# Optimization experiments

Hardware: AMD Instinct MI355X
Metric: run time of the kernel (lower is better)

The kernel has to match this reference:

```python
import jax, jax.numpy as jnp
import numpy as np

D_MODEL, D_K, D_V = 1024, 64, 64
B, S = 4, 4096

def setup_inputs() -> dict:
    key = jax.random.key(0)
    ks = jax.random.split(key, 9)
    s_in = 1.0 / np.sqrt(D_MODEL)
    return {
        "Q": jax.random.normal(ks[0], (B, S, D_MODEL), jnp.float32),
        "K": jax.random.normal(ks[1], (B, S, D_MODEL), jnp.float32),
        "V": jax.random.normal(ks[2], (B, S, D_MODEL), jnp.float32),
        "Wq": jax.random.uniform(ks[3], (D_MODEL, D_K), jnp.float32, -s_in, s_in),
        "bq": jax.random.uniform(ks[4], (D_K,), jnp.float32, -s_in, s_in),
        "Wk": jax.random.uniform(ks[5], (D_MODEL, D_K), jnp.float32, -s_in, s_in),
        "bk": jax.random.uniform(ks[6], (D_K,), jnp.float32, -s_in, s_in),
        "Wv": jax.random.uniform(ks[7], (D_MODEL, D_V), jnp.float32, -s_in, s_in),
        "bv": jax.random.uniform(ks[8], (D_V,), jnp.float32, -s_in, s_in),
    }

def reference(Q, K, V, Wq, bq, Wk, bk, Wv, bv):
    # Linear projections: [B,S,d_model] -> [B,S,d_k/d_v]
    q = jnp.einsum("bsm,mk->bsk", Q, Wq) + bq
    k = jnp.einsum("btm,mk->btk", K, Wk) + bk
    v = jnp.einsum("btm,mv->btv", V, Wv) + bv
    # Scaled dot-product attention, softmax over key axis (dim=2)
    scores = jnp.einsum("bsk,btk->bst", q, k) / jnp.sqrt(jnp.float32(D_K))
    attn = jax.nn.softmax(scores, axis=2)  # [B,S,S]
    return jnp.einsum("bst,btv->bsv", attn, v)
```

## Files before the change

### kernel.cpp

```cpp
#include <hip/hip_runtime.h>

typedef __bf16 bf16;
typedef __attribute__((ext_vector_type(4))) __bf16 bf16x4;
typedef __attribute__((ext_vector_type(8))) __bf16 bf16x8;
typedef __attribute__((ext_vector_type(4))) float f32x4;
typedef __attribute__((ext_vector_type(16))) float f32x16;

#define MFMA16(a, b, c) __builtin_amdgcn_mfma_f32_16x16x32_bf16((a), (b), (c), 0, 0, 0)
#define MFMA32(a, b, c) __builtin_amdgcn_mfma_f32_32x32x16_bf16((a), (b), (c), 0, 0, 0)

__device__ __forceinline__ bf16 tobf(float f) {
    unsigned u = __float_as_uint(f);
    u += 0x7fffu + ((u >> 16) & 1u);
    unsigned short h = (unsigned short)(u >> 16);
    bf16 r;
    __builtin_memcpy(&r, &h, 2);
    return r;
}

__global__ void wconv_kernel(const float* __restrict__ Wq, const float* __restrict__ Wk,
                             const float* __restrict__ Wv, bf16* __restrict__ Wt) {
    int j = blockIdx.y;
    const float* W = (j == 0) ? Wq : ((j == 1) ? Wk : Wv);
    int idx = blockIdx.x * 256 + threadIdx.x;
    int m = idx >> 6, n = idx & 63;
    Wt[(size_t)j * 65536 + (size_t)n * 1024 + m] = tobf(W[idx]);
}

__launch_bounds__(256, 3)
__global__ void proj_kernel(const float* __restrict__ Q, const float* __restrict__ K,
                            const float* __restrict__ V, const bf16* __restrict__ Wt,
                            const float* __restrict__ bq, const float* __restrict__ bk,
                            const float* __restrict__ bv,
                            bf16* __restrict__ q_ws, bf16* __restrict__ k_ws,
                            bf16* __restrict__ vT_ws) {
    const int j = blockIdx.y;
    const float* In   = (j == 0) ? Q : ((j == 1) ? K : V);
    const float* bias = (j == 0) ? bq : ((j == 1) ? bk : bv);
    const bf16* W = Wt + (size_t)j * 65536;

    __shared__ bf16 As[64][136];
    __shared__ bf16 Bs[64][136];

    const int tid = threadIdx.x;
    const int wave = tid >> 6, lane = tid & 63;
    const int quad = lane >> 4, l16 = lane & 15;
    const int rbase = blockIdx.x * 64;

    int arow[8], ag[8];
    const float* apt[8];
#pragma unroll
    for (int i = 0; i < 8; i++) {
        int u = i * 256 + tid;
        arow[i] = u >> 5; ag[i] = u & 31;
        apt[i] = In + (size_t)(rbase + arow[i]) * 1024 + ag[i] * 4;
    }
    int brow[4], bg[4];
    const bf16* bpt[4];
#pragma unroll
    for (int i = 0; i < 4; i++) {
        int u = i * 256 + tid;
        brow[i] = u >> 4; bg[i] = u & 15;
        bpt[i] = W + (size_t)brow[i] * 1024 + bg[i] * 8;
    }

    f32x4 abuf[8];
    bf16x8 bbuf[4];
#pragma unroll
    for (int i = 0; i < 8; i++) abuf[i] = *(const f32x4*)(apt[i]);
#pragma unroll
    for (int i = 0; i < 4; i++) bbuf[i] = *(const bf16x8*)(bpt[i]);

    f32x4 acc[4];
#pragma unroll
    for (int nt = 0; nt < 4; nt++) acc[nt] = {0.f, 0.f, 0.f, 0.f};

#pragma unroll
    for (int it = 0; it < 8; it++) {
#pragma unroll
        for (int i = 0; i < 8; i++) {
            bf16x4 c;
            c[0] = (bf16)abuf[i][0]; c[1] = (bf16)abuf[i][1];
            c[2] = (bf16)abuf[i][2]; c[3] = (bf16)abuf[i][3];
            *(bf16x4*)&As[arow[i]][ag[i] * 4] = c;
        }
#pragma unroll
        for (int i = 0; i < 4; i++) *(bf16x8*)&Bs[brow[i]][bg[i] * 8] = bbuf[i];

        if (it < 7) {
            int kn = (it + 1) * 128;
#pragma unroll
            for (int i = 0; i < 8; i++) abuf[i] = *(const f32x4*)(apt[i] + kn);
#pragma unroll
            for (int i = 0; i < 4; i++) bbuf[i] = *(const bf16x8*)(bpt[i] + kn);
        }
        __syncthreads();

        const int r = wave * 16 + l16;
#pragma unroll
        for (int c = 0; c < 4; c++) {
            bf16x8 av = *(const bf16x8*)&As[r][c * 32 + quad * 8];
#pragma unroll
            for (int nt = 0; nt < 4; nt++) {
                bf16x8 bv = *(const bf16x8*)&Bs[nt * 16 + l16][c * 32 + quad * 8];
                acc[nt] = MFMA16(av, bv, acc[nt]);
            }
        }
        __syncthreads();
    }

    const float scale = (j == 0) ? 0.125f * 1.44269504088896f : 1.0f;

    if (j != 2) {
        bf16* dst = (j == 0) ? q_ws : k_ws;
#pragma unroll
        for (int nt = 0; nt < 4; nt++) {
            int n = nt * 16 + l16;
            float bb = bias[n];
#pragma unroll
            for (int r4 = 0; r4 < 4; r4++) {
                int row = rbase + wave * 16 + quad * 4 + r4;
                dst[(size_t)row * 64 + n] = tobf((acc[nt][r4] + bb) * scale);
            }
        }
    } else {
        bf16 (*vtile)[72] = (bf16(*)[72])As;
#pragma unroll
        for (int nt = 0; nt < 4; nt++) {
            int n = nt * 16 + l16;
            float bb = bias[n];
#pragma unroll
            for (int r4 = 0; r4 < 4; r4++) {
                vtile[n][wave * 16 + quad * 4 + r4] = tobf(acc[nt][r4] + bb);
            }
        }
        __syncthreads();
        int bi = rbase >> 12, t0 = rbase & 4095;
        int d = tid >> 2, part = (tid & 3) * 16;
        bf16x8 x0 = *(const bf16x8*)&vtile[d][part];
        bf16x8 x1 = *(const bf16x8*)&vtile[d][part + 8];
        bf16* dst = vT_ws + (size_t)(bi * 64 + d) * 4096 + t0 + part;
        *(bf16x8*)dst = x0;
        *(bf16x8*)(dst + 8) = x1;
    }
}

__launch_bounds__(256, 4)
__global__ void attn_kernel(const bf16* __restrict__ q_ws, const bf16* __restrict__ k_ws,
                            const bf16* __restrict__ vT_ws,
                            float* __restrict__ po, float* __restrict__ pl,
                            float* __restrict__ out, int keys_per_split, int direct) {
    const int b = blockIdx.z, split = blockIdx.y;
    const int tid = threadIdx.x, wave = tid >> 6, lane = tid & 63;
    const int l32 = lane & 31, h = lane >> 5;
    const int sw = l32 & 7;

    __shared__ bf16 kt[64][64];
    __shared__ bf16 vt[64][64];
    __shared__ bf16 pt[4][32][64];

    const int qrow0 = b * 4096 + blockIdx.x * 128 + wave * 32;

    bf16x8 qf[4];
    const bf16* qp = q_ws + (size_t)(qrow0 + l32) * 64 + h * 8;
#pragma unroll
    for (int c = 0; c < 4; c++) qf[c] = *(const bf16x8*)(qp + c * 16);

    f32x16 o0, o1;
    float l_lane = 0.f;
#pragma unroll
    for (int i = 0; i < 16; i++) { o0[i] = 0.f; o1[i] = 0.f; }

    const int key0 = split * keys_per_split;
    const int srow = tid >> 3;
    const int sg = tid & 7;
    const int sgk = sg ^ (srow & 7);
    const bf16* kg = k_ws + (size_t)(b * 4096 + key0 + srow) * 64 + sg * 8;
    const bf16* vg = vT_ws + (size_t)(b * 64 + srow) * 4096 + key0 + sg * 8;

    uint4 kv0 = *(const uint4*)kg;
    uint4 kv1 = *(const uint4*)(kg + 2048);
    uint4 vv0 = *(const uint4*)vg;
    uint4 vv1 = *(const uint4*)(vg + 131072);

    for (int t0 = 0; t0 < keys_per_split; t0 += 64) {
        __syncthreads();
        *(uint4*)&kt[srow][sgk * 8]      = kv0;
        *(uint4*)&kt[srow + 32][sgk * 8] = kv1;
        *(uint4*)&vt[srow][sgk * 8]      = vv0;
        *(uint4*)&vt[srow + 32][sgk * 8] = vv1;
        if (t0 + 64 < keys_per_split) {
            kv0 = *(const uint4*)(kg + (size_t)(t0 + 64) * 64);
            kv1 = *(const uint4*)(kg + (size_t)(t0 + 64) * 64 + 2048);
            vv0 = *(const uint4*)(vg + t0 + 64);
            vv1 = *(const uint4*)(vg + t0 + 64 + 131072);
        }
        __syncthreads();

#pragma unroll
        for (int kt32 = 0; kt32 < 2; kt32++) {
            f32x16 s;
#pragma unroll
            for (int i = 0; i < 16; i++) s[i] = 0.f;
#pragma unroll
            for (int c = 0; c < 4; c++) {
                bf16x8 kf = *(const bf16x8*)(&kt[kt32 * 32 + l32][((2 * c + h) ^ sw) * 8]);
                s = MFMA32(kf, qf[c], s);
            }
#pragma unroll
            for (int g = 0; g < 4; g++) {
                float p0 = __builtin_amdgcn_exp2f(s[4 * g + 0]);
                float p1 = __builtin_amdgcn_exp2f(s[4 * g + 1]);
                float p2 = __builtin_amdgcn_exp2f(s[4 * g + 2]);
                float p3 = __builtin_amdgcn_exp2f(s[4 * g + 3]);
                l_lane += (p0 + p1) + (p2 + p3);
                bf16x4 pk;
                pk[0] = (bf16)p0; pk[1] = (bf16)p1; pk[2] = (bf16)p2; pk[3] = (bf16)p3;
                int gp = (kt32 * 4 + g) ^ sw;
                *(bf16x4*)(&pt[wave][l32][gp * 8 + 4 * h]) = pk;
            }
        }

#pragma unroll
        for (int tc = 0; tc < 4; tc++) {
            int gp = ((2 * tc + h) ^ sw) * 8;
            bf16x8 pf  = *(const bf16x8*)(&pt[wave][l32][gp]);
            bf16x8 vf0 = *(const bf16x8*)(&vt[l32][gp]);
            bf16x8 vf1 = *(const bf16x8*)(&vt[32 + l32][gp]);
            o0 = MFMA32(pf, vf0, o0);
            o1 = MFMA32(pf, vf1, o1);
        }
    }

    l_lane += __shfl_xor(l_lane, 32);

    if (direct) {
        float* orow = out + (size_t)qrow0 * 64;
#pragma unroll
        for (int i = 0; i < 16; i++) {
            int R = (i & 3) + 8 * (i >> 2) + 4 * h;
            float inv = 1.0f / __shfl(l_lane, R);
            orow[(size_t)R * 64 + l32]      = o0[i] * inv;
            orow[(size_t)R * 64 + 32 + l32] = o1[i] * inv;
        }
    } else {
        size_t prow = (size_t)split * 16384 + qrow0;
        float* pob = po + prow * 64;
#pragma unroll
        for (int i = 0; i < 16; i++) {
            int R = (i & 3) + 8 * (i >> 2) + 4 * h;
            pob[(size_t)R * 64 + l32]      = o0[i];
            pob[(size_t)R * 64 + 32 + l32] = o1[i];
        }
        if (h == 0) pl[prow + l32] = l_lane;
    }
}

__launch_bounds__(256)
__global__ void combine_kernel(const float* __restrict__ po, const float* __restrict__ pl,
                               float* __restrict__ out, int nsplit) {
    int idx = blockIdx.x * 256 + threadIdx.x;
    int row = idx >> 6;
    float so = 0.f, sl = 0.f;
    for (int s = 0; s < nsplit; s++) {
        so += po[(size_t)s * 1048576 + idx];
        sl += pl[(size_t)s * 16384 + row];
    }
    out[idx] = so / sl;
}

extern "C" void kernel_launch(void* const* d_in, const int* in_sizes, int n_in,
                              void* d_out, int out_size, void* d_ws, size_t ws_size,
                              hipStream_t stream) {
    const float* Q  = (const float*)d_in[0];
    const float* K  = (const float*)d_in[1];
    const float* V  = (const float*)d_in[2];
    const float* Wq = (const float*)d_in[3];
    const float* bq = (const float*)d_in[4];
    const float* Wk = (const float*)d_in[5];
    const float* bk = (const float*)d_in[6];
    const float* Wv = (const float*)d_in[7];
    const float* bv = (const float*)d_in[8];
    float* out = (float*)d_out;

    char* ws = (char*)d_ws;
    bf16* Wt    = (bf16*)ws;
    bf16* q_ws  = (bf16*)(ws + 393216);
    bf16* k_ws  = (bf16*)(ws + 393216 + 2097152);
    bf16* vT_ws = (bf16*)(ws + 393216 + 2 * 2097152);
    const size_t base = 393216 + 3 * 2097152;

    const size_t per_split = 16384u * 4u + 1048576u * 4u;
    int nsplit = 1;
    if (ws_size >= base + 8 * per_split) nsplit = 8;
    else if (ws_size >= base + 4 * per_split) nsplit = 4;
    else if (ws_size >= base + 2 * per_split) nsplit = 2;

    float* pl = (float*)(ws + base);
    float* po = (float*)(ws + base + (size_t)nsplit * 65536);

    hipLaunchKernelGGL(wconv_kernel, dim3(256, 3), dim3(256), 0, stream, Wq, Wk, Wv, Wt);
    hipLaunchKernelGGL(proj_kernel, dim3(256, 3), dim3(256), 0, stream,
                       Q, K, V, Wt, bq, bk, bv, q_ws, k_ws, vT_ws);
    hipLaunchKernelGGL(attn_kernel, dim3(32, nsplit, 4), dim3(256), 0, stream,
                       q_ws, k_ws, vT_ws, po, pl, out, 4096 / nsplit, nsplit == 1 ? 1 : 0);
    if (nsplit > 1) {
        hipLaunchKernelGGL(combine_kernel, dim3(4096), dim3(256), 0, stream, po, pl, out, nsplit);
    }
}
```

Before: 246.3 us.

## Load projection A operand straight into MFMA registers and double-buffer weights

In the projection kernel, each lane now loads its own fp32 input row slice from global memory, converts it to bf16 and feeds it directly to the MFMA. The activation tile no longer goes through shared memory. The weight tile is double-buffered in LDS, so one barrier per k-iteration can be dropped. The launch-bounds occupancy hint rises from 3 to 4. This cuts LDS traffic and barrier stalls, at the cost of less regular global access patterns and tighter register pressure.

```diff
diff --git a/kernel.cpp b/kernel.cpp
--- a/kernel.cpp
+++ b/kernel.cpp
@@ -27,7 +27,7 @@
     Wt[(size_t)j * 65536 + (size_t)n * 1024 + m] = tobf(W[idx]);
 }
 
-__launch_bounds__(256, 3)
+__launch_bounds__(256, 4)
 __global__ void proj_kernel(const float* __restrict__ Q, const float* __restrict__ K,
                             const float* __restrict__ V, const bf16* __restrict__ Wt,
                             const float* __restrict__ bq, const float* __restrict__ bk,
@@ -39,22 +39,16 @@
     const float* bias = (j == 0) ? bq : ((j == 1) ? bk : bv);
     const bf16* W = Wt + (size_t)j * 65536;
 
-    __shared__ bf16 As[64][136];
-    __shared__ bf16 Bs[64][136];
+    __shared__ bf16 Bs[2][64][136];
 
     const int tid = threadIdx.x;
     const int wave = tid >> 6, lane = tid & 63;
     const int quad = lane >> 4, l16 = lane & 15;
     const int rbase = blockIdx.x * 64;
-
-    int arow[8], ag[8];
-    const float* apt[8];
-#pragma unroll
-    for (int i = 0; i < 8; i++) {
-        int u = i * 256 + tid;
-        arow[i] = u >> 5; ag[i] = u & 31;
-        apt[i] = In + (size_t)(rbase + arow[i]) * 1024 + ag[i] * 4;
-    }
+    const int myrow = rbase + wave * 16 + l16;
+
+    const float* abase = In + (size_t)myrow * 1024 + quad * 8;
+
     int brow[4], bg[4];
     const bf16* bpt[4];
 #pragma unroll
@@ -64,49 +58,57 @@
         bpt[i] = W + (size_t)brow[i] * 1024 + bg[i] * 8;
     }
 
-    f32x4 abuf[8];
+    f32x4 an[8];
+#pragma unroll
+    for (int c = 0; c < 4; c++) {
+        an[2 * c]     = *(const f32x4*)(abase + c * 32);
+        an[2 * c + 1] = *(const f32x4*)(abase + c * 32 + 4);
+    }
     bf16x8 bbuf[4];
 #pragma unroll
-    for (int i = 0; i < 8; i++) abuf[i] = *(const f32x4*)(apt[i]);
-#pragma unroll
     for (int i = 0; i < 4; i++) bbuf[i] = *(const bf16x8*)(bpt[i]);
 
     f32x4 acc[4];
 #pragma unroll
     for (int nt = 0; nt < 4; nt++) acc[nt] = {0.f, 0.f, 0.f, 0.f};
 
+    bf16x8 acur[4];
+
 #pragma unroll
     for (int it = 0; it < 8; it++) {
 #pragma unroll
-        for (int i = 0; i < 8; i++) {
-            bf16x4 c;
-            c[0] = (bf16)abuf[i][0]; c[1] = (bf16)abuf[i][1];
-            c[2] = (bf16)abuf[i][2]; c[3] = (bf16)abuf[i][3];
-            *(bf16x4*)&As[arow[i]][ag[i] * 4] = c;
-        }
-#pragma unroll
-        for (int i = 0; i < 4; i++) *(bf16x8*)&Bs[brow[i]][bg[i] * 8] = bbuf[i];
-
+        for (int c = 0; c < 4; c++) {
+            bf16x8 v;
+            v[0] = (bf16)an[2 * c][0];     v[1] = (bf16)an[2 * c][1];
+            v[2] = (bf16)an[2 * c][2];     v[3] = (bf16)an[2 * c][3];
+            v[4] = (bf16)an[2 * c + 1][0]; v[5] = (bf16)an[2 * c + 1][1];
+            v[6] = (bf16)an[2 * c + 1][2]; v[7] = (bf16)an[2 * c + 1][3];
+            acur[c] = v;
+        }
         if (it < 7) {
-            int kn = (it + 1) * 128;
-#pragma unroll
-            for (int i = 0; i < 8; i++) abuf[i] = *(const f32x4*)(apt[i] + kn);
-#pragma unroll
-            for (int i = 0; i < 4; i++) bbuf[i] = *(const bf16x8*)(bpt[i] + kn);
+            const float* ap = abase + (it + 1) * 128;
+#pragma unroll
+            for (int c = 0; c < 4; c++) {
+                an[2 * c]     = *(const f32x4*)(ap + c * 32);
+                an[2 * c + 1] = *(const f32x4*)(ap + c * 32 + 4);
+            }
+        }
+#pragma unroll
+        for (int i = 0; i < 4; i++) *(bf16x8*)&Bs[it & 1][brow[i]][bg[i] * 8] = bbuf[i];
+        if (it < 7) {
+#pragma unroll
+            for (int i = 0; i < 4; i++) bbuf[i] = *(const bf16x8*)(bpt[i] + (it + 1) * 128);
         }
         __syncthreads();
 
-        const int r = wave * 16 + l16;
 #pragma unroll
         for (int c = 0; c < 4; c++) {
-            bf16x8 av = *(const bf16x8*)&As[r][c * 32 + quad * 8];
 #pragma unroll
             for (int nt = 0; nt < 4; nt++) {
-                bf16x8 bv = *(const bf16x8*)&Bs[nt * 16 + l16][c * 32 + quad * 8];
-                acc[nt] = MFMA16(av, bv, acc[nt]);
-            }
-        }
-        __syncthreads();
+                bf16x8 bv = *(const bf16x8*)&Bs[it & 1][nt * 16 + l16][c * 32 + quad * 8];
+                acc[nt] = MFMA16(acur[c], bv, acc[nt]);
+            }
+        }
     }
 
     const float scale = (j == 0) ? 0.125f * 1.44269504088896f : 1.0f;
@@ -124,7 +126,7 @@
             }
         }
     } else {
-        bf16 (*vtile)[72] = (bf16(*)[72])As;
+        bf16 (*vtile)[72] = (bf16(*)[72])Bs;
 #pragma unroll
         for (int nt = 0; nt < 4; nt++) {
             int n = nt * 16 + l16;
```

Measured after the change: 243.6 us. About the same (-1.1%).

## Stream projection inputs into double-buffered swizzled LDS via global_load_lds

Applied to the files above, without the earlier changes.

The projection kernel no longer loads fp32 inputs into registers, converts them and writes bf16 to LDS. It now copies fp32 tiles straight into a double-buffered, XOR-swizzled LDS area with global_load_lds, prefetching the next K slice while the current one is computed, and converts to bf16 when reading fragments. Weight fragments are read directly from global/L2 instead of being staged in LDS. This aims to overlap the memory-bound input stream with compute and cut register and VALU staging work. In exchange it uses more LDS per block and issues more global weight loads. Correctness depends on the barrier waiting for the async LDS loads.

```diff
diff --git a/kernel.cpp b/kernel.cpp
--- a/kernel.cpp
+++ b/kernel.cpp
@@ -16,6 +16,12 @@
     bf16 r;
     __builtin_memcpy(&r, &h, 2);
     return r;
+}
+
+__device__ __forceinline__ void stage16(const void* g, void* l) {
+    __builtin_amdgcn_global_load_lds(
+        (const __attribute__((address_space(1))) unsigned int*)g,
+        (__attribute__((address_space(3))) unsigned int*)l, 16, 0, 0);
 }
 
 __global__ void wconv_kernel(const float* __restrict__ Wq, const float* __restrict__ Wk,
@@ -39,72 +45,66 @@
     const float* bias = (j == 0) ? bq : ((j == 1) ? bk : bv);
     const bf16* W = Wt + (size_t)j * 65536;
 
-    __shared__ bf16 As[64][136];
-    __shared__ bf16 Bs[64][136];
+    __shared__ float As[2][64][64];
 
     const int tid = threadIdx.x;
     const int wave = tid >> 6, lane = tid & 63;
     const int quad = lane >> 4, l16 = lane & 15;
     const int rbase = blockIdx.x * 64;
 
-    int arow[8], ag[8];
-    const float* apt[8];
-#pragma unroll
-    for (int i = 0; i < 8; i++) {
-        int u = i * 256 + tid;
-        arow[i] = u >> 5; ag[i] = u & 31;
-        apt[i] = In + (size_t)(rbase + arow[i]) * 1024 + ag[i] * 4;
-    }
-    int brow[4], bg[4];
-    const bf16* bpt[4];
+    const char* asrc[4];
+    char* adst0[4];
+    char* adst1[4];
 #pragma unroll
     for (int i = 0; i < 4; i++) {
         int u = i * 256 + tid;
-        brow[i] = u >> 4; bg[i] = u & 15;
-        bpt[i] = W + (size_t)brow[i] * 1024 + bg[i] * 8;
-    }
-
-    f32x4 abuf[8];
-    bf16x8 bbuf[4];
-#pragma unroll
-    for (int i = 0; i < 8; i++) abuf[i] = *(const f32x4*)(apt[i]);
-#pragma unroll
-    for (int i = 0; i < 4; i++) bbuf[i] = *(const bf16x8*)(bpt[i]);
+        int row = u >> 4;
+        int rg = ((u & 15) * 16) ^ ((row & 7) << 4);
+        asrc[i] = (const char*)(In + (size_t)(rbase + row) * 1024) + rg;
+        adst0[i] = (char*)&As[0][0][0] + u * 16;
+        adst1[i] = (char*)&As[1][0][0] + u * 16;
+    }
+
+#pragma unroll
+    for (int i = 0; i < 4; i++) stage16(asrc[i], adst0[i]);
+    __syncthreads();
 
     f32x4 acc[4];
 #pragma unroll
     for (int nt = 0; nt < 4; nt++) acc[nt] = {0.f, 0.f, 0.f, 0.f};
 
-#pragma unroll
-    for (int it = 0; it < 8; it++) {
-#pragma unroll
-        for (int i = 0; i < 8; i++) {
-            bf16x4 c;
-            c[0] = (bf16)abuf[i][0]; c[1] = (bf16)abuf[i][1];
-            c[2] = (bf16)abuf[i][2]; c[3] = (bf16)abuf[i][3];
-            *(bf16x4*)&As[arow[i]][ag[i] * 4] = c;
-        }
-#pragma unroll
-        for (int i = 0; i < 4; i++) *(bf16x8*)&Bs[brow[i]][bg[i] * 8] = bbuf[i];
-
-        if (it < 7) {
-            int kn = (it + 1) * 128;
-#pragma unroll
-            for (int i = 0; i < 8; i++) abuf[i] = *(const f32x4*)(apt[i] + kn);
-#pragma unroll
-            for (int i = 0; i < 4; i++) bbuf[i] = *(const bf16x8*)(bpt[i] + kn);
-        }
-        __syncthreads();
-
-        const int r = wave * 16 + l16;
-#pragma unroll
-        for (int c = 0; c < 4; c++) {
-            bf16x8 av = *(const bf16x8*)&As[r][c * 32 + quad * 8];
-#pragma unroll
-            for (int nt = 0; nt < 4; nt++) {
-                bf16x8 bv = *(const bf16x8*)&Bs[nt * 16 + l16][c * 32 + quad * 8];
-                acc[nt] = MFMA16(av, bv, acc[nt]);
-            }
+    const int row = wave * 16 + l16;
+    const char* arow = (const char*)&As[0][row][0];
+    const int sw = (l16 & 7) << 4;
+    const bf16* wrow = W + quad * 8;
+
+#pragma unroll 2
+    for (int t = 0; t < 16; ++t) {
+        const int cur = t & 1;
+        if (t < 15) {
+#pragma unroll
+            for (int i = 0; i < 4; i++)
+                stage16(asrc[i] + (t + 1) * 256, cur ? adst0[i] : adst1[i]);
+        }
+        bf16x8 bf[2][4];
+#pragma unroll
+        for (int c = 0; c < 2; c++)
+#pragma unroll
+            for (int nt = 0; nt < 4; nt++)
+                bf[c][nt] = *(const bf16x8*)(wrow + (size_t)(nt * 16 + l16) * 1024 +
+                                             t * 64 + c * 32);
+        const char* ab = arow + (size_t)cur * 16384;
+#pragma unroll
+        for (int c = 0; c < 2; c++) {
+            f32x4 a0 = *(const f32x4*)(ab + ((c * 128 + quad * 32) ^ sw));
+            f32x4 a1 = *(const f32x4*)(ab + ((c * 128 + quad * 32 + 16) ^ sw));
+            bf16x8 av;
+            av[0] = (bf16)a0[0]; av[1] = (bf16)a0[1];
+            av[2] = (bf16)a0[2]; av[3] = (bf16)a0[3];
+            av[4] = (bf16)a1[0]; av[5] = (bf16)a1[1];
+            av[6] = (bf16)a1[2]; av[7] = (bf16)a1[3];
+#pragma unroll
+            for (int nt = 0; nt < 4; nt++) acc[nt] = MFMA16(av, bf[c][nt], acc[nt]);
         }
         __syncthreads();
     }
@@ -119,8 +119,8 @@
             float bb = bias[n];
 #pragma unroll
             for (int r4 = 0; r4 < 4; r4++) {
-                int row = rbase + wave * 16 + quad * 4 + r4;
-                dst[(size_t)row * 64 + n] = tobf((acc[nt][r4] + bb) * scale);
+                int orow = rbase + wave * 16 + quad * 4 + r4;
+                dst[(size_t)orow * 64 + n] = tobf((acc[nt][r4] + bb) * scale);
             }
         }
     } else {
```

New measurement: 254.4 us. 3.3% more time.
